# Optimization experiments

Measured on AMD Instinct MI355X. Metric: run time of the kernel, lower is better.

The kernel has to match this reference:

```python
import jax, jax.numpy as jnp
import numpy as np

A = 32        # num_agents (nodes per graph block)
B = 128       # batch graphs
N = B * A     # nodes per timestep = 4096
T = 5         # temporal_window_size
K = 16        # num_belief_states
AD = 8        # action_dim
H = 4         # num_attn_heads
DH = 64       # hidden_dim (per GAT head)
D = H * DH    # feature_dim = 256
HD = D // H   # temporal MHA head dim = 64
L = 64        # latent_dim
FIN = K + AD  # discrete node feature dim = 24


def _block_edges():
    # fully connected within each batch block, incl. self loops (PyG GATConv default)
    s = np.repeat(np.arange(A), A)
    d = np.tile(np.arange(A), A)
    off = (np.arange(B) * A)[:, None]
    src = (off + s[None, :]).reshape(-1)
    dst = (off + d[None, :]).reshape(-1)
    return jnp.asarray(np.stack([src, dst]), dtype=jnp.int32)  # [2, B*A*A]


def setup_inputs():
    key = jax.random.key(0)
    ks = jax.random.split(key, 16)
    g = lambda i, shape, s=0.05: jax.random.normal(ks[i], shape, dtype=jnp.float32) * s
    z = lambda shape: jnp.zeros(shape, jnp.float32)
    return {
        'node_feats': g(0, (T, N, FIN), 1.0),
        'edge_index': _block_edges(),
        'gat1_w': g(1, (FIN, D)), 'gat1_asrc': g(2, (H, DH)), 'gat1_adst': g(3, (H, DH)), 'gat1_b': z((D,)),
        'gat2_w': g(4, (D, D)), 'gat2_asrc': g(5, (H, DH)), 'gat2_adst': g(6, (H, DH)), 'gat2_b': z((D,)),
        'wq': g(7, (D, D)), 'bq': z((D,)),
        'wk': g(8, (D, D)), 'bk': z((D,)),
        'wv': g(9, (D, D)), 'bv': z((D,)),
        'wo': g(10, (D, D)), 'bo': z((D,)),
        'lm_w': g(11, (D, L)), 'lm_b': z((L,)),
        'lv_w': g(12, (D, L)), 'lv_b': z((L,)),
        'ap_w': g(13, (L, AD * A)), 'ap_b': z((AD * A,)),
        'bh_w': g(14, (D, K)), 'bh_b': z((K,)),
    }


def _gat_layer(x, W, a_src, a_dst, b, src, dst):
    # PyG GATConv: per-edge additive attention, softmax over incoming edges of dst
    h = (x @ W).reshape(N, H, DH)
    al_s = (h * a_src[None]).sum(-1)                      # [N,H]
    al_d = (h * a_dst[None]).sum(-1)                      # [N,H]
    e = jax.nn.leaky_relu(al_s[src] + al_d[dst], 0.2)     # [E,H]
    m = jax.ops.segment_max(e, dst, num_segments=N)
    p = jnp.exp(e - m[dst])
    zden = jax.ops.segment_sum(p, dst, num_segments=N)
    alpha = p / (zden[dst] + 1e-16)                       # [E,H]
    out = jax.ops.segment_sum(h[src] * alpha[:, :, None], dst, num_segments=N)
    return out.reshape(N, D) + b


def reference(node_feats, edge_index, gat1_w, gat1_asrc, gat1_adst, gat1_b,
              gat2_w, gat2_asrc, gat2_adst, gat2_b,
              wq, bq, wk, bk, wv, bv, wo, bo,
              lm_w, lm_b, lv_w, lv_b, ap_w, ap_b, bh_w, bh_b):
    src, dst = edge_index[0], edge_index[1]

    def gnn(x):  # two GATConv layers + ReLU (dropout inactive at inference)
        x = jax.nn.relu(_gat_layer(x, gat1_w, gat1_asrc, gat1_adst, gat1_b, src, dst))
        x = jax.nn.relu(_gat_layer(x, gat2_w, gat2_asrc, gat2_adst, gat2_b, src, dst))
        return x

    feats = jax.vmap(gnn)(node_feats)          # [T,N,D]
    ego = feats[:, ::A, :]                     # ego node of each block -> [T,B,D]
    seq = jnp.transpose(ego, (1, 0, 2))        # [B,T,D]

    # temporal MultiheadAttention with causal mask (batch_first)
    q = (seq @ wq + bq).reshape(B, T, H, HD)
    k = (seq @ wk + bk).reshape(B, T, H, HD)
    v = (seq @ wv + bv).reshape(B, T, H, HD)
    scores = jnp.einsum('bthd,bshd->bhts', q, k) / jnp.sqrt(jnp.float32(HD))
    causal = jnp.tril(jnp.ones((T, T), bool))
    scores = jnp.where(causal[None, None], scores, jnp.float32(-1e9))
    attn = jax.nn.softmax(scores, axis=-1)
    ctx = jnp.einsum('bhts,bshd->bthd', attn, v).reshape(B, T, D)
    feat = (ctx @ wo + bo)[:, -1]              # last timestep features [B,D]

    mu = feat @ lm_w + lm_b                    # latent_mean
    logvar = feat @ lv_w + lv_b                # latent_logvar
    act = mu @ ap_w + ap_b                     # action_predictor(latent)
    belief = feat @ bh_w + bh_b                # belief_head(features)
    return jnp.concatenate([mu, logvar, act, belief], axis=-1)  # [B, 2L+AD*A+K]
```

## Files before the change

### kernel.cpp

```cpp
#include <hip/hip_runtime.h>

typedef unsigned short u16;
typedef unsigned int u32;
typedef short bf16x8 __attribute__((ext_vector_type(8)));
typedef float f32x4  __attribute__((ext_vector_type(4)));


__device__ __forceinline__ u16 f2b(float f) {
    unsigned u = __float_as_uint(f);
    return (u16)((u + 0x7FFFu + ((u >> 16) & 1u)) >> 16);
}
__device__ __forceinline__ float b2f(u16 u) {
    return __uint_as_float(((unsigned)u) << 16);
}

__global__ __launch_bounds__(256) void prep_w2_kernel(
    const float* __restrict__ w, u16* __restrict__ wt)
{
    __shared__ float tile[32][33];
    const int bi = blockIdx.x >> 3, bj = blockIdx.x & 7;
    const int r0 = bi * 32, c0 = bj * 32;
    const int lr = threadIdx.x >> 5, lc = threadIdx.x & 31;
    for (int i = lr; i < 32; i += 8)
        tile[i][lc] = w[(r0 + i) * 256 + c0 + lc];
    __syncthreads();
    for (int i = lr; i < 32; i += 8)
        wt[(c0 + i) * 256 + r0 + lc] = f2b(tile[lc][i]);
}

__global__ __launch_bounds__(256, 3) void gat12_kernel(
    const float* __restrict__ x,
    const float* __restrict__ w1, const float* __restrict__ a1s,
    const float* __restrict__ a1d, const float* __restrict__ b1,
    const u16* __restrict__ w2t, const float* __restrict__ a2s,
    const float* __restrict__ a2d, const float* __restrict__ b2,
    u16* __restrict__ ego,
    const float* __restrict__ wq, const float* __restrict__ wk,
    const float* __restrict__ wv, const float* __restrict__ wo,
    const float* __restrict__ lm_w, const float* __restrict__ lv_w,
    const float* __restrict__ bh_w, const float* __restrict__ ap_w,
    u16* __restrict__ wqkvt, u16* __restrict__ wot,
    u16* __restrict__ headT, u16* __restrict__ apT)
{
    constexpr int FIN = 24;
    constexpr int HP = 40;
    constexpr int XP = 264;

    __shared__ u16 h1T[256 * HP];
    __shared__ u16 x2s[32 * XP];
    __shared__ u16 alphaT[4 * 32 * HP];
    __shared__ float als2[256], ald2[256];
    __shared__ float a1sf[256], a1df[256], a2sf[256], a2df[256];
    __shared__ float alpha0[4][32];

    const int tid = threadIdx.x;

    if (blockIdx.x >= 640) {
        const int bid = blockIdx.x - 640;
        const float* src; u16* dst;
        int C = 256, S = 256, roff = 0, bi, bj;
        if (bid < 192) {
            const int m = bid >> 6, tl = bid & 63;
            src = (m == 0) ? wq : (m == 1) ? wk : wv;
            dst = wqkvt + m * 65536;
            bi = tl >> 3; bj = tl & 7;
        } else if (bid < 256) {
            const int tl = bid - 192;
            src = wo; dst = wot; bi = tl >> 3; bj = tl & 7;
        } else if (bid < 272) {
            const int tl = bid - 256;
            src = lm_w; dst = headT; C = 64; bi = tl >> 1; bj = tl & 1;
        } else if (bid < 288) {
            const int tl = bid - 272;
            src = lv_w; dst = headT; C = 64; roff = 64; bi = tl >> 1; bj = tl & 1;
        } else if (bid < 296) {
            src = bh_w; dst = headT; C = 16; roff = 128; bi = bid - 288; bj = 0;
        } else {
            const int tl = bid - 296;
            src = ap_w; dst = apT; S = 64; bi = tl >> 3; bj = tl & 7;
        }
        float (*tile)[33] = (float(*)[33])h1T;
        const int r0 = bi * 32, c0 = bj * 32;
        const int lr = tid >> 5, lc = tid & 31;
        const int cw = (C - c0 < 32) ? (C - c0) : 32;
        for (int i = lr; i < 32; i += 8)
            if (lc < cw) tile[i][lc] = src[(r0 + i) * C + c0 + lc];
        __syncthreads();
        for (int i = lr; i < cw; i += 8)
            dst[(roff + c0 + i) * S + r0 + lc] = f2b(tile[lc][i]);
        return;
    }

    const int wave = tid >> 6;
    const int l    = tid & 63;
    const int l15  = l & 15;
    const int quad = l >> 4;
    const int t    = blockIdx.x >> 7;
    const int b    = blockIdx.x & 127;
    const long row0 = (long)(t * 4096 + b * 32);

    float* xst = (float*)alphaT;
    if (tid < 192) {
        const float4 v = *(const float4*)(x + row0 * FIN + tid * 4);
        const int r = tid / 6, c = (tid % 6) * 4;
        *(float4*)&xst[r * 28 + c] = v;
    }
    a1sf[tid] = a1s[tid];  a1df[tid] = a1d[tid];
    a2sf[tid] = a2s[tid];  a2df[tid] = a2d[tid];
    __syncthreads();

    {
        float acc[32];
#pragma unroll
        for (int i = 0; i < 32; ++i) acc[i] = 0.f;
        for (int k0 = 0; k0 < FIN; k0 += 4) {
            const float w0 = w1[(k0 + 0) * 256 + tid];
            const float wA = w1[(k0 + 1) * 256 + tid];
            const float wB = w1[(k0 + 2) * 256 + tid];
            const float wC = w1[(k0 + 3) * 256 + tid];
#pragma unroll
            for (int i = 0; i < 32; ++i) {
                const float4 xv = *(const float4*)&xst[i * 28 + k0];
                acc[i] += xv.x * w0 + xv.y * wA + xv.z * wB + xv.w * wC;
            }
        }
        __syncthreads();
        u32 pk[16];
#pragma unroll
        for (int s = 0; s < 16; ++s)
            pk[s] = (u32)f2b(acc[2 * s]) | ((u32)f2b(acc[2 * s + 1]) << 16);
        u32* dst = (u32*)&h1T[tid * HP];
#pragma unroll
        for (int s = 0; s < 4; ++s)
            *(uint4*)&dst[s * 4] = make_uint4(pk[4*s], pk[4*s+1], pk[4*s+2], pk[4*s+3]);
    }
    __syncthreads();

    {
        const int pair = tid >> 7;
        const int id = tid & 127;
        const int i = id >> 2, hh = id & 3;
        float as = 0.f, ad = 0.f;
        for (int cc = 0; cc < 32; ++cc) {
            const int c = (((cc + tid) & 31) | (pair << 5)) + hh * 64;
            const float hv = b2f(h1T[c * HP + i]);
            as += hv * a1sf[c];
            ad += hv * a1df[c];
        }
        als2[tid] = as;
        ald2[tid] = ad;
    }
    __syncthreads();

    if (tid < 128) {
        const int hh = tid & 3, dd = tid >> 2;
        const float advv = ald2[tid] + ald2[128 + tid];
        float e[32]; float m = -1e30f;
#pragma unroll
        for (int s = 0; s < 32; ++s) {
            float v = (als2[s * 4 + hh] + als2[128 + s * 4 + hh]) + advv;
            v = v > 0.f ? v : 0.2f * v;
            e[s] = v; m = fmaxf(m, v);
        }
        float sum = 0.f;
#pragma unroll
        for (int s = 0; s < 32; ++s) { float p = __expf(e[s] - m); e[s] = p; sum += p; }
        const float inv = 1.f / (sum + 1e-16f);
        u32 pk[16];
#pragma unroll
        for (int s = 0; s < 16; ++s)
            pk[s] = (u32)f2b(e[2*s] * inv) | ((u32)f2b(e[2*s+1] * inv) << 16);
        u32* dst = (u32*)&alphaT[(hh * 32 + dd) * HP];
#pragma unroll
        for (int s = 0; s < 4; ++s)
            *(uint4*)&dst[s * 4] = make_uint4(pk[4*s], pk[4*s+1], pk[4*s+2], pk[4*s+3]);
    }
    __syncthreads();

    {
        const int hh = wave;
        bf16x8 af[2];
#pragma unroll
        for (int mt = 0; mt < 2; ++mt)
            af[mt] = *(const bf16x8*)&alphaT[(hh * 32 + mt * 16 + l15) * HP + quad * 8];
        f32x4 acc[2][4];
#pragma unroll
        for (int mt = 0; mt < 2; ++mt)
#pragma unroll
            for (int nt = 0; nt < 4; ++nt) acc[mt][nt] = (f32x4){0.f, 0.f, 0.f, 0.f};
#pragma unroll
        for (int nt = 0; nt < 4; ++nt) {
            const bf16x8 bf = *(const bf16x8*)&h1T[(hh * 64 + nt * 16 + l15) * HP + quad * 8];
            acc[0][nt] = __builtin_amdgcn_mfma_f32_16x16x32_bf16(af[0], bf, acc[0][nt], 0, 0, 0);
            acc[1][nt] = __builtin_amdgcn_mfma_f32_16x16x32_bf16(af[1], bf, acc[1][nt], 0, 0, 0);
        }
#pragma unroll
        for (int mt = 0; mt < 2; ++mt)
#pragma unroll
            for (int nt = 0; nt < 4; ++nt) {
                const int col = hh * 64 + nt * 16 + l15;
                const float bb = b1[col];
#pragma unroll
                for (int r = 0; r < 4; ++r) {
                    const int d = mt * 16 + quad * 4 + r;
                    x2s[d * XP + col] = f2b(fmaxf(acc[mt][nt][r] + bb, 0.f));
                }
            }
    }
    __syncthreads();

    u16* h2s = h1T;
    {
        const int n0 = wave * 64;
        f32x4 acc[2][4];
#pragma unroll
        for (int mt = 0; mt < 2; ++mt)
#pragma unroll
            for (int nt = 0; nt < 4; ++nt) acc[mt][nt] = (f32x4){0.f, 0.f, 0.f, 0.f};
        for (int k0 = 0; k0 < 256; k0 += 32) {
            const int kb = k0 + quad * 8;
            const bf16x8 a0 = *(const bf16x8*)&x2s[(l15)      * XP + kb];
            const bf16x8 a1 = *(const bf16x8*)&x2s[(16 + l15) * XP + kb];
#pragma unroll
            for (int nt = 0; nt < 4; ++nt) {
                const bf16x8 bb = *(const bf16x8*)(w2t + (n0 + nt * 16 + l15) * 256 + kb);
                acc[0][nt] = __builtin_amdgcn_mfma_f32_16x16x32_bf16(a0, bb, acc[0][nt], 0, 0, 0);
                acc[1][nt] = __builtin_amdgcn_mfma_f32_16x16x32_bf16(a1, bb, acc[1][nt], 0, 0, 0);
            }
        }
        __syncthreads();
#pragma unroll
        for (int mt = 0; mt < 2; ++mt)
#pragma unroll
            for (int nt = 0; nt < 4; ++nt)
#pragma unroll
                for (int r = 0; r < 4; ++r)
                    h2s[(mt * 16 + quad * 4 + r) * XP + n0 + nt * 16 + l15] =
                        f2b(acc[mt][nt][r]);
    }
    __syncthreads();

    {
        const int pair = tid >> 7;
        const int id = tid & 127;
        const int i = id >> 2, hh = id & 3;
        float as = 0.f, ad = 0.f;
        for (int cc = 0; cc < 32; ++cc) {
            const int c = (((cc + tid) & 31) | (pair << 5)) + hh * 64;
            const float hv = b2f(h2s[i * XP + c]);
            as += hv * a2sf[c];
            ad += hv * a2df[c];
        }
        als2[tid] = as;
        ald2[tid] = ad;
    }
    __syncthreads();

    if (tid < 4) {
        const int hh = tid;
        const float advv = ald2[hh] + ald2[128 + hh];
        float e[32]; float m = -1e30f;
#pragma unroll
        for (int s = 0; s < 32; ++s) {
            float v = (als2[s * 4 + hh] + als2[128 + s * 4 + hh]) + advv;
            v = v > 0.f ? v : 0.2f * v;
            e[s] = v; m = fmaxf(m, v);
        }
        float sum = 0.f;
#pragma unroll
        for (int s = 0; s < 32; ++s) { float p = __expf(e[s] - m); e[s] = p; sum += p; }
        const float inv = 1.f / (sum + 1e-16f);
#pragma unroll
        for (int s = 0; s < 32; ++s) alpha0[hh][s] = e[s] * inv;
    }
    __syncthreads();

    {
        const int hh = tid >> 6;
        float a = 0.f;
#pragma unroll
        for (int s = 0; s < 32; ++s)
            a += alpha0[hh][s] * b2f(h2s[s * XP + tid]);
        ego[((long)(t * 128 + b)) * 256 + tid] = f2b(fmaxf(a + b2[tid], 0.f));
    }
}

__global__ __launch_bounds__(256) void qkv_kernel(
    const u16* __restrict__ ego, const u16* __restrict__ wqkvt,
    const float* __restrict__ bq, const float* __restrict__ bk,
    const float* __restrict__ bv_, float* __restrict__ qkv)
{
    const int tid  = threadIdx.x;
    const int wave = tid >> 6;
    const int l    = tid & 63;
    const int l15  = l & 15;
    const int quad = l >> 4;
    int gx, gy;
    if (blockIdx.x < 20)      { gy = 1; gx = blockIdx.x; }
    else if (blockIdx.x < 40) { gy = 2; gx = blockIdx.x - 20; }
    else                      { gy = 0; gx = 16 + (blockIdx.x - 40); }
    const int r0 = gx * 32;
    const int n0 = wave * 64;
    const u16* wsrc = wqkvt + gy * 65536;
    const float* bias = (gy == 0) ? bq : (gy == 1) ? bk : bv_;

    f32x4 acc[2][4];
#pragma unroll
    for (int mt = 0; mt < 2; ++mt)
#pragma unroll
        for (int nt = 0; nt < 4; ++nt) acc[mt][nt] = (f32x4){0.f, 0.f, 0.f, 0.f};

    for (int k0 = 0; k0 < 256; k0 += 32) {
        const int kb = k0 + quad * 8;
        const bf16x8 a0 = *(const bf16x8*)(ego + (r0 + l15)      * 256 + kb);
        const bf16x8 a1 = *(const bf16x8*)(ego + (r0 + 16 + l15) * 256 + kb);
#pragma unroll
        for (int nt = 0; nt < 4; ++nt) {
            const bf16x8 bb = *(const bf16x8*)(wsrc + (n0 + nt * 16 + l15) * 256 + kb);
            acc[0][nt] = __builtin_amdgcn_mfma_f32_16x16x32_bf16(a0, bb, acc[0][nt], 0, 0, 0);
            acc[1][nt] = __builtin_amdgcn_mfma_f32_16x16x32_bf16(a1, bb, acc[1][nt], 0, 0, 0);
        }
    }
#pragma unroll
    for (int mt = 0; mt < 2; ++mt)
#pragma unroll
        for (int nt = 0; nt < 4; ++nt)
#pragma unroll
            for (int r = 0; r < 4; ++r) {
                const int row = r0 + mt * 16 + quad * 4 + r;
                const int col = n0 + nt * 16 + l15;
                qkv[(long)row * 768 + gy * 256 + col] = acc[mt][nt][r] + bias[col];
            }
}

__global__ __launch_bounds__(256) void attn_kernel(
    const float* __restrict__ qkv, u16* __restrict__ ctx_g)
{
    __shared__ float q4[256], kk[5 * 256], vv[5 * 256];
    __shared__ float scl[20], attw[20];

    const int j = threadIdx.x;
    const int b = blockIdx.x;

    q4[j] = qkv[(long)(512 + b) * 768 + j];
#pragma unroll
    for (int t = 0; t < 5; ++t) {
        const long r = (long)(t * 128 + b) * 768;
        kk[t * 256 + j] = qkv[r + 256 + j];
        vv[t * 256 + j] = qkv[r + 512 + j];
    }
    __syncthreads();

    if (j < 20) {
        const int hh = j / 5, ss = j % 5;
        float sc = 0.f;
        for (int c = 0; c < 64; ++c)
            sc += q4[hh * 64 + c] * kk[ss * 256 + hh * 64 + c];
        scl[j] = sc * 0.125f;
    }
    __syncthreads();

    if (j < 4) {
        float m = -1e30f;
        for (int ss = 0; ss < 5; ++ss) m = fmaxf(m, scl[j * 5 + ss]);
        float p[5], sum = 0.f;
        for (int ss = 0; ss < 5; ++ss) { p[ss] = __expf(scl[j * 5 + ss] - m); sum += p[ss]; }
        for (int ss = 0; ss < 5; ++ss) attw[j * 5 + ss] = p[ss] / sum;
    }
    __syncthreads();

    {
        const int hh = j >> 6;
        float c = 0.f;
#pragma unroll
        for (int ss = 0; ss < 5; ++ss) c += attw[hh * 5 + ss] * vv[ss * 256 + j];
        ctx_g[b * 256 + j] = f2b(c);
    }
}

__global__ __launch_bounds__(256) void tail_kernel(
    const u16* __restrict__ ctx_g, const u16* __restrict__ wot,
    const u16* __restrict__ headT, const u16* __restrict__ apT,
    const float* __restrict__ bo,
    const float* __restrict__ lm_b, const float* __restrict__ lv_b,
    const float* __restrict__ bh_b, const float* __restrict__ ap_b,
    float* __restrict__ out)
{
    constexpr int FP = 264;
    constexpr int MP = 72;
    __shared__ u16 fs[32 * FP];
    __shared__ u16 mus[32 * MP];

    const int tid  = threadIdx.x;
    const int wave = tid >> 6;
    const int l    = tid & 63;
    const int l15  = l & 15;
    const int quad = l >> 4;
    const int r0   = blockIdx.x * 32;

    {
        const int n0 = wave * 64;
        f32x4 acc[2][4];
#pragma unroll
        for (int mt = 0; mt < 2; ++mt)
#pragma unroll
            for (int nt = 0; nt < 4; ++nt) acc[mt][nt] = (f32x4){0.f, 0.f, 0.f, 0.f};
        for (int k0 = 0; k0 < 256; k0 += 32) {
            const int kb = k0 + quad * 8;
            const bf16x8 a0 = *(const bf16x8*)(ctx_g + (r0 + l15)      * 256 + kb);
            const bf16x8 a1 = *(const bf16x8*)(ctx_g + (r0 + 16 + l15) * 256 + kb);
#pragma unroll
            for (int nt = 0; nt < 4; ++nt) {
                const bf16x8 bb = *(const bf16x8*)(wot + (n0 + nt * 16 + l15) * 256 + kb);
                acc[0][nt] = __builtin_amdgcn_mfma_f32_16x16x32_bf16(a0, bb, acc[0][nt], 0, 0, 0);
                acc[1][nt] = __builtin_amdgcn_mfma_f32_16x16x32_bf16(a1, bb, acc[1][nt], 0, 0, 0);
            }
        }
#pragma unroll
        for (int mt = 0; mt < 2; ++mt)
#pragma unroll
            for (int nt = 0; nt < 4; ++nt) {
                const int col = n0 + nt * 16 + l15;
                const float bb = bo[col];
#pragma unroll
                for (int r = 0; r < 4; ++r)
                    fs[(mt * 16 + quad * 4 + r) * FP + col] = f2b(acc[mt][nt][r] + bb);
            }
    }
    __syncthreads();

    for (int nt = wave; nt < 9; nt += 4) {
        const int n0 = nt * 16;
        f32x4 acc[2];
        acc[0] = (f32x4){0.f, 0.f, 0.f, 0.f};
        acc[1] = (f32x4){0.f, 0.f, 0.f, 0.f};
        for (int k0 = 0; k0 < 256; k0 += 32) {
            const int kb = k0 + quad * 8;
            const bf16x8 a0 = *(const bf16x8*)&fs[(l15)      * FP + kb];
            const bf16x8 a1 = *(const bf16x8*)&fs[(16 + l15) * FP + kb];
            const bf16x8 bb = *(const bf16x8*)(headT + (n0 + l15) * 256 + kb);
            acc[0] = __builtin_amdgcn_mfma_f32_16x16x32_bf16(a0, bb, acc[0], 0, 0, 0);
            acc[1] = __builtin_amdgcn_mfma_f32_16x16x32_bf16(a1, bb, acc[1], 0, 0, 0);
        }
        const int col = n0 + l15;
#pragma unroll
        for (int mt = 0; mt < 2; ++mt)
#pragma unroll
            for (int r = 0; r < 4; ++r) {
                const int row = mt * 16 + quad * 4 + r;
                float v = acc[mt][r];
                if (col < 64) {
                    v += lm_b[col];
                    out[(long)(r0 + row) * 400 + col] = v;
                    mus[row * MP + col] = f2b(v);
                } else if (col < 128) {
                    v += lv_b[col - 64];
                    out[(long)(r0 + row) * 400 + col] = v;
                } else {
                    v += bh_b[col - 128];
                    out[(long)(r0 + row) * 400 + 256 + col] = v;
                }
            }
    }
    __syncthreads();

    {
#pragma unroll
        for (int i = 0; i < 4; ++i) {
            const int n0 = (wave * 4 + i) * 16;
            f32x4 acc[2];
            acc[0] = (f32x4){0.f, 0.f, 0.f, 0.f};
            acc[1] = (f32x4){0.f, 0.f, 0.f, 0.f};
#pragma unroll
            for (int k0 = 0; k0 < 64; k0 += 32) {
                const int kb = k0 + quad * 8;
                const bf16x8 a0 = *(const bf16x8*)&mus[(l15)      * MP + kb];
                const bf16x8 a1 = *(const bf16x8*)&mus[(16 + l15) * MP + kb];
                const bf16x8 bb = *(const bf16x8*)(apT + (n0 + l15) * 64 + kb);
                acc[0] = __builtin_amdgcn_mfma_f32_16x16x32_bf16(a0, bb, acc[0], 0, 0, 0);
                acc[1] = __builtin_amdgcn_mfma_f32_16x16x32_bf16(a1, bb, acc[1], 0, 0, 0);
            }
            const int col = n0 + l15;
            const float bb = ap_b[col];
#pragma unroll
            for (int mt = 0; mt < 2; ++mt)
#pragma unroll
                for (int r = 0; r < 4; ++r) {
                    const int row = mt * 16 + quad * 4 + r;
                    out[(long)(r0 + row) * 400 + 128 + col] = acc[mt][r] + bb;
                }
        }
    }
}

extern "C" void kernel_launch(void* const* d_in, const int* in_sizes, int n_in,
                              void* d_out, int out_size, void* d_ws, size_t ws_size,
                              hipStream_t stream)
{
    const float* node_feats = (const float*)d_in[0];
    const float* g1w  = (const float*)d_in[2];
    const float* g1as = (const float*)d_in[3];
    const float* g1ad = (const float*)d_in[4];
    const float* g1b  = (const float*)d_in[5];
    const float* g2w  = (const float*)d_in[6];
    const float* g2as = (const float*)d_in[7];
    const float* g2ad = (const float*)d_in[8];
    const float* g2b  = (const float*)d_in[9];
    const float* wq = (const float*)d_in[10]; const float* bq = (const float*)d_in[11];
    const float* wk = (const float*)d_in[12]; const float* bk = (const float*)d_in[13];
    const float* wv = (const float*)d_in[14]; const float* bv = (const float*)d_in[15];
    const float* wo = (const float*)d_in[16]; const float* bo = (const float*)d_in[17];
    const float* lm_w = (const float*)d_in[18]; const float* lm_b = (const float*)d_in[19];
    const float* lv_w = (const float*)d_in[20]; const float* lv_b = (const float*)d_in[21];
    const float* ap_w = (const float*)d_in[22]; const float* ap_b = (const float*)d_in[23];
    const float* bh_w = (const float*)d_in[24]; const float* bh_b = (const float*)d_in[25];

    char* ws = (char*)d_ws;
    u16*   ego   = (u16*)ws;
    u16*   w2t   = (u16*)(ws + 327680);
    u16*   wqkvt = (u16*)(ws + 458752);
    float* qkv   = (float*)(ws + 851968);
    u16*   wot   = (u16*)(ws + 2818048);
    u16*   headT = (u16*)(ws + 2949120);
    u16*   apT   = (u16*)(ws + 3022848);
    u16*   ctx_g = (u16*)(ws + 3055616);

    prep_w2_kernel<<<64, 256, 0, stream>>>(g2w, w2t);
    gat12_kernel<<<952, 256, 0, stream>>>(node_feats, g1w, g1as, g1ad, g1b,
                                          w2t, g2as, g2ad, g2b, ego,
                                          wq, wk, wv, wo, lm_w, lv_w, bh_w, ap_w,
                                          wqkvt, wot, headT, apT);
    qkv_kernel<<<44, 256, 0, stream>>>(ego, wqkvt, bq, bk, bv, qkv);
    attn_kernel<<<128, 256, 0, stream>>>(qkv, ctx_g);
    tail_kernel<<<4, 256, 0, stream>>>(ctx_g, wot, headT, apT, bo,
                                       lm_b, lv_b, bh_b, ap_b, (float*)d_out);
}
```

Before: 164.1 us.

## Use MFMA for GAT layer-1, fuse attention into tail kernel, transpose h2 layout

Layer-1 projection now runs as bf16 MFMA using a pre-transposed, zero-padded bf16 copy of W1 built in the prep kernel, replacing the scalar FMA loop. The temporal attention kernel is merged into the tail kernel, now 8 blocks of 16 graphs, which removes one launch and the ctx round trip through global memory. The h2 tile is stored transposed with packed stores. Attention vectors are kept as bf16 in LDS, and the dst logit is computed only for the ego row. Together these aim to cut launch overhead and scalar work, at the cost of extra bf16 rounding of x and the attention vectors.

```diff
diff --git a/kernel.cpp b/kernel.cpp
--- a/kernel.cpp
+++ b/kernel.cpp
@@ -13,25 +13,45 @@
 __device__ __forceinline__ float b2f(u16 u) {
     return __uint_as_float(((unsigned)u) << 16);
 }
-
-__global__ __launch_bounds__(256) void prep_w2_kernel(
-    const float* __restrict__ w, u16* __restrict__ wt)
+__device__ __forceinline__ u32 pk2(float a, float b) {
+    return (u32)f2b(a) | ((u32)f2b(b) << 16);
+}
+
+__global__ __launch_bounds__(256) void prep_kernel(
+    const float* __restrict__ w2, u16* __restrict__ w2t,
+    const float* __restrict__ w1, u16* __restrict__ w1t)
 {
+    if (blockIdx.x == 64) {
+        const int n = threadIdx.x;
+        u32 pk[16];
+#pragma unroll
+        for (int s = 0; s < 16; ++s) {
+            const int k = 2 * s;
+            const float lo = (k < 24)     ? w1[k * 256 + n]       : 0.f;
+            const float hi = (k + 1 < 24) ? w1[(k + 1) * 256 + n] : 0.f;
+            pk[s] = pk2(lo, hi);
+        }
+        u32* dst = (u32*)(w1t + n * 32);
+#pragma unroll
+        for (int s = 0; s < 4; ++s)
+            *(uint4*)&dst[s * 4] = make_uint4(pk[4*s], pk[4*s+1], pk[4*s+2], pk[4*s+3]);
+        return;
+    }
     __shared__ float tile[32][33];
     const int bi = blockIdx.x >> 3, bj = blockIdx.x & 7;
     const int r0 = bi * 32, c0 = bj * 32;
     const int lr = threadIdx.x >> 5, lc = threadIdx.x & 31;
     for (int i = lr; i < 32; i += 8)
-        tile[i][lc] = w[(r0 + i) * 256 + c0 + lc];
+        tile[i][lc] = w2[(r0 + i) * 256 + c0 + lc];
     __syncthreads();
     for (int i = lr; i < 32; i += 8)
-        wt[(c0 + i) * 256 + r0 + lc] = f2b(tile[lc][i]);
+        w2t[(c0 + i) * 256 + r0 + lc] = f2b(tile[lc][i]);
 }
 
 __global__ __launch_bounds__(256, 3) void gat12_kernel(
-    const float* __restrict__ x,
-    const float* __restrict__ w1, const float* __restrict__ a1s,
-    const float* __restrict__ a1d, const float* __restrict__ b1,
+    const float* __restrict__ x, const u16* __restrict__ w1t,
+    const float* __restrict__ a1s, const float* __restrict__ a1d,
+    const float* __restrict__ b1,
     const u16* __restrict__ w2t, const float* __restrict__ a2s,
     const float* __restrict__ a2d, const float* __restrict__ b2,
     u16* __restrict__ ego,
@@ -42,7 +62,6 @@
     u16* __restrict__ wqkvt, u16* __restrict__ wot,
     u16* __restrict__ headT, u16* __restrict__ apT)
 {
-    constexpr int FIN = 24;
     constexpr int HP = 40;
     constexpr int XP = 264;
 
@@ -50,7 +69,7 @@
     __shared__ u16 x2s[32 * XP];
     __shared__ u16 alphaT[4 * 32 * HP];
     __shared__ float als2[256], ald2[256];
-    __shared__ float a1sf[256], a1df[256], a2sf[256], a2df[256];
+    __shared__ u16 a1sb[256], a1db[256], a2sb[256], a2db[256];
     __shared__ float alpha0[4][32];
 
     const int tid = threadIdx.x;
@@ -99,40 +118,44 @@
     const int b    = blockIdx.x & 127;
     const long row0 = (long)(t * 4096 + b * 32);
 
-    float* xst = (float*)alphaT;
-    if (tid < 192) {
-        const float4 v = *(const float4*)(x + row0 * FIN + tid * 4);
-        const int r = tid / 6, c = (tid % 6) * 4;
-        *(float4*)&xst[r * 28 + c] = v;
-    }
-    a1sf[tid] = a1s[tid];  a1df[tid] = a1d[tid];
-    a2sf[tid] = a2s[tid];  a2df[tid] = a2d[tid];
-    __syncthreads();
-
-    {
-        float acc[32];
-#pragma unroll
-        for (int i = 0; i < 32; ++i) acc[i] = 0.f;
-        for (int k0 = 0; k0 < FIN; k0 += 4) {
-            const float w0 = w1[(k0 + 0) * 256 + tid];
-            const float wA = w1[(k0 + 1) * 256 + tid];
-            const float wB = w1[(k0 + 2) * 256 + tid];
-            const float wC = w1[(k0 + 3) * 256 + tid];
-#pragma unroll
-            for (int i = 0; i < 32; ++i) {
-                const float4 xv = *(const float4*)&xst[i * 28 + k0];
-                acc[i] += xv.x * w0 + xv.y * wA + xv.z * wB + xv.w * wC;
-            }
+    u16* xs = alphaT;
+    if (tid < 128) {
+        const int node = tid >> 2, seg = tid & 3;
+        u32 pk[4] = {0, 0, 0, 0};
+        if (seg < 3) {
+            const float* xp = x + row0 * 24 + node * 24 + seg * 8;
+            const float4 v0 = *(const float4*)xp;
+            const float4 v1 = *(const float4*)(xp + 4);
+            pk[0] = pk2(v0.x, v0.y); pk[1] = pk2(v0.z, v0.w);
+            pk[2] = pk2(v1.x, v1.y); pk[3] = pk2(v1.z, v1.w);
+        }
+        *(uint4*)&xs[node * 32 + seg * 8] = make_uint4(pk[0], pk[1], pk[2], pk[3]);
+    }
+    a1sb[tid] = f2b(a1s[tid]);  a1db[tid] = f2b(a1d[tid]);
+    a2sb[tid] = f2b(a2s[tid]);  a2db[tid] = f2b(a2d[tid]);
+    __syncthreads();
+
+    {
+        const int n0 = wave * 64;
+        const bf16x8 a0 = *(const bf16x8*)&xs[(l15)      * 32 + quad * 8];
+        const bf16x8 a1 = *(const bf16x8*)&xs[(16 + l15) * 32 + quad * 8];
+        f32x4 acc[2][4];
+#pragma unroll
+        for (int nt = 0; nt < 4; ++nt) {
+            const bf16x8 bb = *(const bf16x8*)(w1t + (n0 + nt * 16 + l15) * 32 + quad * 8);
+            acc[0][nt] = __builtin_amdgcn_mfma_f32_16x16x32_bf16(a0, bb, (f32x4){0.f,0.f,0.f,0.f}, 0, 0, 0);
+            acc[1][nt] = __builtin_amdgcn_mfma_f32_16x16x32_bf16(a1, bb, (f32x4){0.f,0.f,0.f,0.f}, 0, 0, 0);
         }
         __syncthreads();
-        u32 pk[16];
-#pragma unroll
-        for (int s = 0; s < 16; ++s)
-            pk[s] = (u32)f2b(acc[2 * s]) | ((u32)f2b(acc[2 * s + 1]) << 16);
-        u32* dst = (u32*)&h1T[tid * HP];
-#pragma unroll
-        for (int s = 0; s < 4; ++s)
-            *(uint4*)&dst[s * 4] = make_uint4(pk[4*s], pk[4*s+1], pk[4*s+2], pk[4*s+3]);
+#pragma unroll
+        for (int mt = 0; mt < 2; ++mt)
+#pragma unroll
+            for (int nt = 0; nt < 4; ++nt) {
+                const int col = n0 + nt * 16 + l15;
+                *(uint2*)&h1T[col * HP + mt * 16 + quad * 4] =
+                    make_uint2(pk2(acc[mt][nt][0], acc[mt][nt][1]),
+                               pk2(acc[mt][nt][2], acc[mt][nt][3]));
+            }
     }
     __syncthreads();
 
@@ -144,8 +167,8 @@
         for (int cc = 0; cc < 32; ++cc) {
             const int c = (((cc + tid) & 31) | (pair << 5)) + hh * 64;
             const float hv = b2f(h1T[c * HP + i]);
-            as += hv * a1sf[c];
-            ad += hv * a1df[c];
+            as += hv * b2f(a1sb[c]);
+            ad += hv * b2f(a1db[c]);
         }
         als2[tid] = as;
         ald2[tid] = ad;
@@ -168,8 +191,7 @@
         const float inv = 1.f / (sum + 1e-16f);
         u32 pk[16];
 #pragma unroll
-        for (int s = 0; s < 16; ++s)
-            pk[s] = (u32)f2b(e[2*s] * inv) | ((u32)f2b(e[2*s+1] * inv) << 16);
+        for (int s = 0; s < 16; ++s) pk[s] = pk2(e[2*s] * inv, e[2*s+1] * inv);
         u32* dst = (u32*)&alphaT[(hh * 32 + dd) * HP];
 #pragma unroll
         for (int s = 0; s < 4; ++s)
@@ -228,15 +250,15 @@
                 acc[1][nt] = __builtin_amdgcn_mfma_f32_16x16x32_bf16(a1, bb, acc[1][nt], 0, 0, 0);
             }
         }
-        __syncthreads();
 #pragma unroll
         for (int mt = 0; mt < 2; ++mt)
 #pragma unroll
-            for (int nt = 0; nt < 4; ++nt)
-#pragma unroll
-                for (int r = 0; r < 4; ++r)
-                    h2s[(mt * 16 + quad * 4 + r) * XP + n0 + nt * 16 + l15] =
-                        f2b(acc[mt][nt][r]);
+            for (int nt = 0; nt < 4; ++nt) {
+                const int col = n0 + nt * 16 + l15;
+                *(uint2*)&h2s[col * HP + mt * 16 + quad * 4] =
+                    make_uint2(pk2(acc[mt][nt][0], acc[mt][nt][1]),
+                               pk2(acc[mt][nt][2], acc[mt][nt][3]));
+            }
     }
     __syncthreads();
 
@@ -247,12 +269,12 @@
         float as = 0.f, ad = 0.f;
         for (int cc = 0; cc < 32; ++cc) {
             const int c = (((cc + tid) & 31) | (pair << 5)) + hh * 64;
-            const float hv = b2f(h2s[i * XP + c]);
-            as += hv * a2sf[c];
-            ad += hv * a2df[c];
+            const float hv = b2f(h2s[c * HP + i]);
+            as += hv * b2f(a2sb[c]);
+            if (i == 0) ad += hv * b2f(a2db[c]);
         }
         als2[tid] = as;
-        ald2[tid] = ad;
+        if (i == 0) ald2[tid] = ad;
     }
     __syncthreads();
 
@@ -277,10 +299,18 @@
 
     {
         const int hh = tid >> 6;
+        float av[32];
+#pragma unroll
+        for (int j = 0; j < 8; ++j)
+            *(float4*)&av[j * 4] = *(const float4*)&alpha0[hh][j * 4];
+        const u32* hp = (const u32*)&h2s[tid * HP];
         float a = 0.f;
 #pragma unroll
-        for (int s = 0; s < 32; ++s)
-            a += alpha0[hh][s] * b2f(h2s[s * XP + tid]);
+        for (int s2 = 0; s2 < 16; ++s2) {
+            const u32 u = hp[s2];
+            a += av[2 * s2]     * __uint_as_float(u << 16);
+            a += av[2 * s2 + 1] * __uint_as_float(u & 0xffff0000u);
+        }
         ego[((long)(t * 128 + b)) * 256 + tid] = f2b(fmaxf(a + b2[tid], 0.f));
     }
 }
@@ -333,54 +363,10 @@
             }
 }
 
-__global__ __launch_bounds__(256) void attn_kernel(
-    const float* __restrict__ qkv, u16* __restrict__ ctx_g)
-{
-    __shared__ float q4[256], kk[5 * 256], vv[5 * 256];
-    __shared__ float scl[20], attw[20];
-
-    const int j = threadIdx.x;
-    const int b = blockIdx.x;
-
-    q4[j] = qkv[(long)(512 + b) * 768 + j];
-#pragma unroll
-    for (int t = 0; t < 5; ++t) {
-        const long r = (long)(t * 128 + b) * 768;
-        kk[t * 256 + j] = qkv[r + 256 + j];
-        vv[t * 256 + j] = qkv[r + 512 + j];
-    }
-    __syncthreads();
-
-    if (j < 20) {
-        const int hh = j / 5, ss = j % 5;
-        float sc = 0.f;
-        for (int c = 0; c < 64; ++c)
-            sc += q4[hh * 64 + c] * kk[ss * 256 + hh * 64 + c];
-        scl[j] = sc * 0.125f;
-    }
-    __syncthreads();
-
-    if (j < 4) {
-        float m = -1e30f;
-        for (int ss = 0; ss < 5; ++ss) m = fmaxf(m, scl[j * 5 + ss]);
-        float p[5], sum = 0.f;
-        for (int ss = 0; ss < 5; ++ss) { p[ss] = __expf(scl[j * 5 + ss] - m); sum += p[ss]; }
-        for (int ss = 0; ss < 5; ++ss) attw[j * 5 + ss] = p[ss] / sum;
-    }
-    __syncthreads();
-
-    {
-        const int hh = j >> 6;
-        float c = 0.f;
-#pragma unroll
-        for (int ss = 0; ss < 5; ++ss) c += attw[hh * 5 + ss] * vv[ss * 256 + j];
-        ctx_g[b * 256 + j] = f2b(c);
-    }
-}
-
-__global__ __launch_bounds__(256) void tail_kernel(
-    const u16* __restrict__ ctx_g, const u16* __restrict__ wot,
-    const u16* __restrict__ headT, const u16* __restrict__ apT,
+__global__ __launch_bounds__(256) void attn_tail_kernel(
+    const float* __restrict__ qkv,
+    const u16* __restrict__ wot, const u16* __restrict__ headT,
+    const u16* __restrict__ apT,
     const float* __restrict__ bo,
     const float* __restrict__ lm_b, const float* __restrict__ lv_b,
     const float* __restrict__ bh_b, const float* __restrict__ ap_b,
@@ -388,107 +374,125 @@
 {
     constexpr int FP = 264;
     constexpr int MP = 72;
-    __shared__ u16 fs[32 * FP];
-    __shared__ u16 mus[32 * MP];
+    __shared__ float scl[16][20];
+    __shared__ u16 fs[16 * FP];
+    __shared__ u16 ffs[16 * FP];
+    __shared__ u16 mus[16 * MP];
 
     const int tid  = threadIdx.x;
     const int wave = tid >> 6;
     const int l    = tid & 63;
     const int l15  = l & 15;
     const int quad = l >> 4;
-    const int r0   = blockIdx.x * 32;
+    const int b0   = blockIdx.x * 16;
+
+    for (int id = tid; id < 320; id += 256) {
+        const int bl = id / 20, r = id % 20, h = r / 5, s = r % 5;
+        const float* qp = qkv + (long)(512 + b0 + bl) * 768 + h * 64;
+        const float* kp = qkv + (long)(s * 128 + b0 + bl) * 768 + 256 + h * 64;
+        float acc = 0.f;
+        for (int c = 0; c < 64; c += 4) {
+            const float4 qv = *(const float4*)(qp + c);
+            const float4 kv = *(const float4*)(kp + c);
+            acc += qv.x * kv.x + qv.y * kv.y + qv.z * kv.z + qv.w * kv.w;
+        }
+        scl[bl][r] = acc * 0.125f;
+    }
+    __syncthreads();
+
+    if (tid < 64) {
+        const int bl = tid >> 2, h = tid & 3;
+        float m = -1e30f;
+        for (int s = 0; s < 5; ++s) m = fmaxf(m, scl[bl][h * 5 + s]);
+        float p[5], sum = 0.f;
+        for (int s = 0; s < 5; ++s) { p[s] = __expf(scl[bl][h * 5 + s] - m); sum += p[s]; }
+        for (int s = 0; s < 5; ++s) scl[bl][h * 5 + s] = p[s] / sum;
+    }
+    __syncthreads();
+
+    {
+        const int col = tid, h = col >> 6;
+        for (int bl = 0; bl < 16; ++bl) {
+            float c = 0.f;
+#pragma unroll
+            for (int s = 0; s < 5; ++s)
+                c += scl[bl][h * 5 + s] * qkv[(long)(s * 128 + b0 + bl) * 768 + 512 + col];
+            fs[bl * FP + col] = f2b(c);
+        }
+    }
+    __syncthreads();
 
     {
         const int n0 = wave * 64;
-        f32x4 acc[2][4];
-#pragma unroll
-        for (int mt = 0; mt < 2; ++mt)
-#pragma unroll
-            for (int nt = 0; nt < 4; ++nt) acc[mt][nt] = (f32x4){0.f, 0.f, 0.f, 0.f};
+        f32x4 acc[4];
+#pragma unroll
+        for (int nt = 0; nt < 4; ++nt) acc[nt] = (f32x4){0.f, 0.f, 0.f, 0.f};
         for (int k0 = 0; k0 < 256; k0 += 32) {
             const int kb = k0 + quad * 8;
-            const bf16x8 a0 = *(const bf16x8*)(ctx_g + (r0 + l15)      * 256 + kb);
-            const bf16x8 a1 = *(const bf16x8*)(ctx_g + (r0 + 16 + l15) * 256 + kb);
+            const bf16x8 a = *(const bf16x8*)&fs[l15 * FP + kb];
 #pragma unroll
             for (int nt = 0; nt < 4; ++nt) {
                 const bf16x8 bb = *(const bf16x8*)(wot + (n0 + nt * 16 + l15) * 256 + kb);
-                acc[0][nt] = __builtin_amdgcn_mfma_f32_16x16x32_bf16(a0, bb, acc[0][nt], 0, 0, 0);
-                acc[1][nt] = __builtin_amdgcn_mfma_f32_16x16x32_bf16(a1, bb, acc[1][nt], 0, 0, 0);
-            }
-        }
-#pragma unroll
-        for (int mt = 0; mt < 2; ++mt)
-#pragma unroll
-            for (int nt = 0; nt < 4; ++nt) {
-                const int col = n0 + nt * 16 + l15;
-                const float bb = bo[col];
-#pragma unroll
-                for (int r = 0; r < 4; ++r)
-                    fs[(mt * 16 + quad * 4 + r) * FP + col] = f2b(acc[mt][nt][r] + bb);
-            }
+                acc[nt] = __builtin_amdgcn_mfma_f32_16x16x32_bf16(a, bb, acc[nt], 0, 0, 0);
+            }
+        }
+#pragma unroll
+        for (int nt = 0; nt < 4; ++nt) {
+            const int col = n0 + nt * 16 + l15;
+            const float bb = bo[col];
+#pragma unroll
+            for (int r = 0; r < 4; ++r)
+                ffs[(quad * 4 + r) * FP + col] = f2b(acc[nt][r] + bb);
+        }
     }
     __syncthreads();
 
     for (int nt = wave; nt < 9; nt += 4) {
         const int n0 = nt * 16;
-        f32x4 acc[2];
-        acc[0] = (f32x4){0.f, 0.f, 0.f, 0.f};
-        acc[1] = (f32x4){0.f, 0.f, 0.f, 0.f};
+        f32x4 acc = (f32x4){0.f, 0.f, 0.f, 0.f};
         for (int k0 = 0; k0 < 256; k0 += 32) {
             const int kb = k0 + quad * 8;
-            const bf16x8 a0 = *(const bf16x8*)&fs[(l15)      * FP + kb];
-            const bf16x8 a1 = *(const bf16x8*)&fs[(16 + l15) * FP + kb];
+            const bf16x8 a  = *(const bf16x8*)&ffs[l15 * FP + kb];
             const bf16x8 bb = *(const bf16x8*)(headT + (n0 + l15) * 256 + kb);
-            acc[0] = __builtin_amdgcn_mfma_f32_16x16x32_bf16(a0, bb, acc[0], 0, 0, 0);
-            acc[1] = __builtin_amdgcn_mfma_f32_16x16x32_bf16(a1, bb, acc[1], 0, 0, 0);
+            acc = __builtin_amdgcn_mfma_f32_16x16x32_bf16(a, bb, acc, 0, 0, 0);
         }
         const int col = n0 + l15;
 #pragma unroll
-        for (int mt = 0; mt < 2; ++mt)
-#pragma unroll
-            for (int r = 0; r < 4; ++r) {
-                const int row = mt * 16 + quad * 4 + r;
-                float v = acc[mt][r];
-                if (col < 64) {
-                    v += lm_b[col];
-                    out[(long)(r0 + row) * 400 + col] = v;
-                    mus[row * MP + col] = f2b(v);
-                } else if (col < 128) {
-                    v += lv_b[col - 64];
-                    out[(long)(r0 + row) * 400 + col] = v;
-                } else {
-                    v += bh_b[col - 128];
-                    out[(long)(r0 + row) * 400 + 256 + col] = v;
-                }
-            }
-    }
-    __syncthreads();
-
-    {
-#pragma unroll
-        for (int i = 0; i < 4; ++i) {
-            const int n0 = (wave * 4 + i) * 16;
-            f32x4 acc[2];
-            acc[0] = (f32x4){0.f, 0.f, 0.f, 0.f};
-            acc[1] = (f32x4){0.f, 0.f, 0.f, 0.f};
-#pragma unroll
-            for (int k0 = 0; k0 < 64; k0 += 32) {
-                const int kb = k0 + quad * 8;
-                const bf16x8 a0 = *(const bf16x8*)&mus[(l15)      * MP + kb];
-                const bf16x8 a1 = *(const bf16x8*)&mus[(16 + l15) * MP + kb];
-                const bf16x8 bb = *(const bf16x8*)(apT + (n0 + l15) * 64 + kb);
-                acc[0] = __builtin_amdgcn_mfma_f32_16x16x32_bf16(a0, bb, acc[0], 0, 0, 0);
-                acc[1] = __builtin_amdgcn_mfma_f32_16x16x32_bf16(a1, bb, acc[1], 0, 0, 0);
-            }
-            const int col = n0 + l15;
-            const float bb = ap_b[col];
-#pragma unroll
-            for (int mt = 0; mt < 2; ++mt)
-#pragma unroll
-                for (int r = 0; r < 4; ++r) {
-                    const int row = mt * 16 + quad * 4 + r;
-                    out[(long)(r0 + row) * 400 + 128 + col] = acc[mt][r] + bb;
-                }
+        for (int r = 0; r < 4; ++r) {
+            const int row = quad * 4 + r;
+            float v = acc[r];
+            if (col < 64) {
+                v += lm_b[col];
+                out[(long)(b0 + row) * 400 + col] = v;
+                mus[row * MP + col] = f2b(v);
+            } else if (col < 128) {
+                v += lv_b[col - 64];
+                out[(long)(b0 + row) * 400 + col] = v;
+            } else {
+                v += bh_b[col - 128];
+                out[(long)(b0 + row) * 400 + 256 + col] = v;
+            }
+        }
+    }
+    __syncthreads();
+
+#pragma unroll
+    for (int i = 0; i < 4; ++i) {
+        const int n0 = (wave * 4 + i) * 16;
+        f32x4 acc = (f32x4){0.f, 0.f, 0.f, 0.f};
+#pragma unroll
+        for (int k0 = 0; k0 < 64; k0 += 32) {
+            const int kb = k0 + quad * 8;
+            const bf16x8 a  = *(const bf16x8*)&mus[l15 * MP + kb];
+            const bf16x8 bb = *(const bf16x8*)(apT + (n0 + l15) * 64 + kb);
+            acc = __builtin_amdgcn_mfma_f32_16x16x32_bf16(a, bb, acc, 0, 0, 0);
+        }
+        const int col = n0 + l15;
+        const float bb = ap_b[col];
+#pragma unroll
+        for (int r = 0; r < 4; ++r) {
+            const int row = quad * 4 + r;
+            out[(long)(b0 + row) * 400 + 128 + col] = acc[r] + bb;
         }
     }
 }
@@ -518,20 +522,19 @@
     char* ws = (char*)d_ws;
     u16*   ego   = (u16*)ws;
     u16*   w2t   = (u16*)(ws + 327680);
-    u16*   wqkvt = (u16*)(ws + 458752);
-    float* qkv   = (float*)(ws + 851968);
-    u16*   wot   = (u16*)(ws + 2818048);
-    u16*   headT = (u16*)(ws + 2949120);
-    u16*   apT   = (u16*)(ws + 3022848);
-    u16*   ctx_g = (u16*)(ws + 3055616);
-
-    prep_w2_kernel<<<64, 256, 0, stream>>>(g2w, w2t);
-    gat12_kernel<<<952, 256, 0, stream>>>(node_feats, g1w, g1as, g1ad, g1b,
+    u16*   w1t   = (u16*)(ws + 458752);
+    u16*   wqkvt = (u16*)(ws + 475136);
+    float* qkv   = (float*)(ws + 868352);
+    u16*   wot   = (u16*)(ws + 2834432);
+    u16*   headT = (u16*)(ws + 2965504);
+    u16*   apT   = (u16*)(ws + 3039232);
+
+    prep_kernel<<<65, 256, 0, stream>>>(g2w, w2t, g1w, w1t);
+    gat12_kernel<<<952, 256, 0, stream>>>(node_feats, w1t, g1as, g1ad, g1b,
                                           w2t, g2as, g2ad, g2b, ego,
                                           wq, wk, wv, wo, lm_w, lv_w, bh_w, ap_w,
                                           wqkvt, wot, headT, apT);
     qkv_kernel<<<44, 256, 0, stream>>>(ego, wqkvt, bq, bk, bv, qkv);
-    attn_kernel<<<128, 256, 0, stream>>>(qkv, ctx_g);
-    tail_kernel<<<4, 256, 0, stream>>>(ctx_g, wot, headT, apT, bo,
-                                       lm_b, lv_b, bh_b, ap_b, (float*)d_out);
-}
+    attn_tail_kernel<<<8, 256, 0, stream>>>(qkv, wot, headT, apT, bo,
+                                            lm_b, lv_b, bh_b, ap_b, (float*)d_out);
+}
```

Result: faster. 156.9 us (-4.4%).
